# Performance work log

Measured on AMD Instinct MI355X. Metric: run time of the kernel, lower is better.

## Reference

```python
import jax, jax.numpy as jnp
import numpy as np

B, D, HW, C = 256, 128, 36, 64  # batch, proj_dim, spatial side, num classes
EPS = 1e-4


def setup_inputs() -> dict:
    key = jax.random.key(0)
    k1, k2 = jax.random.split(key)
    x = jax.random.normal(k1, (B, D, HW, HW), dtype=jnp.float32)
    class_map = jax.random.randint(k2, (B, HW, HW), 0, C, dtype=jnp.int32)
    return {"x": x, "class_map": class_map}


def reference(x, class_map):
    # Faithful to ImageParser.compute_dists: per-image group-by-class mean
    # of pixel embeddings, then per-pixel squared distance to its class mean.
    # torch.unique + one_hot over inv_idxs is equivalent to using the raw
    # class ids as segments (absent classes contribute nothing).
    b, d = x.shape[0], x.shape[1]
    n = x.shape[2] * x.shape[3]            # 36*36 = 1296
    xf = x.reshape(b, d, n)                # [B, D, N]
    cm = class_map.reshape(b, n)           # [B, N]

    onehot = jax.nn.one_hot(cm, C, dtype=xf.dtype)          # [B, N, C]
    counts = onehot.sum(axis=1)                              # [B, C]
    sums = jnp.einsum('bdn,bnc->bdc', xf, onehot)            # [B, D, C]
    means = sums / (counts[:, None, :] + EPS)                # [B, D, C]

    # gather each pixel's class mean: means[b, :, cm[b, n]] -> [B, D, N]
    idx = jnp.broadcast_to(cm[:, None, :], (b, d, n))
    gathered = jnp.take_along_axis(means, idx, axis=2)

    dists = ((xf - gathered) ** 2).mean(axis=1)              # [B, N]
    return dists[..., None]                                  # [B, N, 1] as in torch
```

## Files before the change

### kernel.cpp

```cpp
#include <hip/hip_runtime.h>

static constexpr int kB   = 256;
static constexpr int kD   = 128;
static constexpr int kN   = 1296;
static constexpr int kN4  = 324;
static constexpr int kC   = 64;
static constexpr int kDC  = 8;
static constexpr int kNCH = kD / kDC;
static constexpr int kREP = 4;
static constexpr int kT   = 384;
static constexpr float kEPS = 1e-4f;
static constexpr float kSCALE     = 131072.0f;
static constexpr float kINV_SCALE = 1.0f / 131072.0f;

__device__ __forceinline__ void fadd_glb(float* p, float v) { unsafeAtomicAdd(p, v); }

__global__ __launch_bounds__(kT) void k_fused(const float* __restrict__ x,
                                              const int*   __restrict__ cm,
                                              float* __restrict__ out)
{
    __shared__ int   isum_s[kREP][kDC][kC];
    __shared__ float means_s[kDC][kC];
    __shared__ int   cnt_s[kC];

    const int chunk = blockIdx.x;
    const int b     = blockIdx.y;
    const int tid   = threadIdx.x;
    const int rep   = (tid >> 4) & (kREP - 1);
    const int rot   = rep << 3;
    const bool act  = tid < kN4;

    for (int i = tid; i < kREP * kDC * kC; i += kT) (&isum_s[0][0][0])[i] = 0;
    if (tid < kC) cnt_s[tid] = 0;
    __syncthreads();

    int4 c0 = make_int4(0, 0, 0, 0);
    if (act) c0 = ((const int4*)(cm + (size_t)b * kN))[tid];

    const float4* xp = (const float4*)(x + ((size_t)b * kD + (size_t)chunk * kDC) * kN);
    float4 va[kDC];
#pragma unroll
    for (int dd = 0; dd < kDC; ++dd)
        va[dd] = act ? xp[(size_t)dd * kN4 + tid] : make_float4(0.f, 0.f, 0.f, 0.f);

    if (act) {
        atomicAdd(&cnt_s[c0.x], 1);
        atomicAdd(&cnt_s[c0.y], 1);
        atomicAdd(&cnt_s[c0.z], 1);
        atomicAdd(&cnt_s[c0.w], 1);
        const int sx = (c0.x + rot) & (kC - 1);
        const int sy = (c0.y + rot) & (kC - 1);
        const int sz = (c0.z + rot) & (kC - 1);
        const int sw = (c0.w + rot) & (kC - 1);
#pragma unroll
        for (int dd = 0; dd < kDC; ++dd) {
            int* s = &isum_s[rep][dd][0];
            atomicAdd(s + sx, __float2int_rn(va[dd].x * kSCALE));
            atomicAdd(s + sy, __float2int_rn(va[dd].y * kSCALE));
            atomicAdd(s + sz, __float2int_rn(va[dd].z * kSCALE));
            atomicAdd(s + sw, __float2int_rn(va[dd].w * kSCALE));
        }
    }
    __syncthreads();

    for (int i = tid; i < kDC * kC; i += kT) {
        const int dd = i >> 6;
        const int c  = i & (kC - 1);
        int s = isum_s[0][dd][c];
#pragma unroll
        for (int r = 1; r < kREP; ++r)
            s += isum_s[r][dd][(c + (r << 3)) & (kC - 1)];
        means_s[dd][c] = (float)s * kINV_SCALE / ((float)cnt_s[c] + kEPS);
    }
    __syncthreads();

    if (act) {
        float a0 = 0.f, a1 = 0.f, a2 = 0.f, a3 = 0.f;
#pragma unroll
        for (int dd = 0; dd < kDC; ++dd) {
            const float* m = &means_s[dd][0];
            const float d0 = va[dd].x - m[c0.x];
            const float d1 = va[dd].y - m[c0.y];
            const float d2 = va[dd].z - m[c0.z];
            const float d3 = va[dd].w - m[c0.w];
            a0 += d0 * d0; a1 += d1 * d1; a2 += d2 * d2; a3 += d3 * d3;
        }
        const float inv = 1.0f / (float)kD;
        float* ob = out + (size_t)b * kN + 4 * (size_t)tid;
        fadd_glb(ob + 0, a0 * inv);
        fadd_glb(ob + 1, a1 * inv);
        fadd_glb(ob + 2, a2 * inv);
        fadd_glb(ob + 3, a3 * inv);
    }
}

__global__ __launch_bounds__(kT) void k_stream(const float* __restrict__ x,
                                               float* __restrict__ ws)
{
    const int tid = threadIdx.x;
    if (tid >= kN4) return;
    const int chunk = blockIdx.x;
    const int b     = blockIdx.y;
    const float4* xp = (const float4*)(x + ((size_t)b * kD + (size_t)chunk * kDC) * kN);
    float a = 0.f;
#pragma unroll
    for (int dd = 0; dd < kDC; ++dd) {
        const float4 v = xp[(size_t)dd * kN4 + tid];
        a += v.x + v.y + v.z + v.w;
    }
    ws[((size_t)b * kNCH + chunk) * kN4 + tid] = a;
}

extern "C" void kernel_launch(void* const* d_in, const int* in_sizes, int n_in,
                              void* d_out, int out_size, void* d_ws, size_t ws_size,
                              hipStream_t stream) {
    const float* x   = (const float*)d_in[0];
    const int*   cm  = (const int*)d_in[1];
    float*       out = (float*)d_out;
    float*       ws  = (float*)d_ws;

    hipMemsetAsync(d_out, 0, (size_t)out_size * sizeof(float), stream);

    dim3 grid(kNCH, kB);
    k_fused<<<grid, kT, 0, stream>>>(x, cm, out);
    k_stream<<<grid, kT, 0, stream>>>(x, ws);
}
```

Before: 277.1 us.

## Replace global float atomics with per-chunk partials and a reduce kernel; drop redundant stream kernel

The fused kernel now writes its per-chunk squared-distance partials as float4 stores into a workspace buffer instead of doing global float atomic adds. A new small kernel sums the 16 chunk partials and applies the 1/D scale. This removes the output memset, the global atomics, and the extra kernel that re-read all of x into an unused workspace. Shared-memory zeroing is moved after the x loads and vectorised so it can overlap the load latency. The cost is an extra partial buffer write and read plus one more kernel launch.

```diff
diff --git a/kernel.cpp b/kernel.cpp
--- a/kernel.cpp
+++ b/kernel.cpp
@@ -13,11 +13,10 @@
 static constexpr float kSCALE     = 131072.0f;
 static constexpr float kINV_SCALE = 1.0f / 131072.0f;
 
-__device__ __forceinline__ void fadd_glb(float* p, float v) { unsafeAtomicAdd(p, v); }
 
 __global__ __launch_bounds__(kT) void k_fused(const float* __restrict__ x,
                                               const int*   __restrict__ cm,
-                                              float* __restrict__ out)
+                                              float* __restrict__ part)
 {
     __shared__ int   isum_s[kREP][kDC][kC];
     __shared__ float means_s[kDC][kC];
@@ -30,10 +29,6 @@
     const int rot   = rep << 3;
     const bool act  = tid < kN4;
 
-    for (int i = tid; i < kREP * kDC * kC; i += kT) (&isum_s[0][0][0])[i] = 0;
-    if (tid < kC) cnt_s[tid] = 0;
-    __syncthreads();
-
     int4 c0 = make_int4(0, 0, 0, 0);
     if (act) c0 = ((const int4*)(cm + (size_t)b * kN))[tid];
 
@@ -42,6 +37,11 @@
 #pragma unroll
     for (int dd = 0; dd < kDC; ++dd)
         va[dd] = act ? xp[(size_t)dd * kN4 + tid] : make_float4(0.f, 0.f, 0.f, 0.f);
+
+    int4* z = (int4*)&isum_s[0][0][0];
+    for (int i = tid; i < (kREP * kDC * kC) / 4; i += kT) z[i] = make_int4(0, 0, 0, 0);
+    if (tid < kC) cnt_s[tid] = 0;
+    __syncthreads();
 
     if (act) {
         atomicAdd(&cnt_s[c0.x], 1);
@@ -85,43 +85,41 @@
             const float d3 = va[dd].w - m[c0.w];
             a0 += d0 * d0; a1 += d1 * d1; a2 += d2 * d2; a3 += d3 * d3;
         }
-        const float inv = 1.0f / (float)kD;
-        float* ob = out + (size_t)b * kN + 4 * (size_t)tid;
-        fadd_glb(ob + 0, a0 * inv);
-        fadd_glb(ob + 1, a1 * inv);
-        fadd_glb(ob + 2, a2 * inv);
-        fadd_glb(ob + 3, a3 * inv);
+        float4 o; o.x = a0; o.y = a1; o.z = a2; o.w = a3;
+        float* pb = part + ((size_t)chunk * kB + b) * kN;
+        ((float4*)pb)[tid] = o;
     }
 }
 
-__global__ __launch_bounds__(kT) void k_stream(const float* __restrict__ x,
-                                               float* __restrict__ ws)
+__global__ __launch_bounds__(256) void k_reduce(const float* __restrict__ part,
+                                                float* __restrict__ out)
 {
-    const int tid = threadIdx.x;
-    if (tid >= kN4) return;
-    const int chunk = blockIdx.x;
-    const int b     = blockIdx.y;
-    const float4* xp = (const float4*)(x + ((size_t)b * kD + (size_t)chunk * kDC) * kN);
-    float a = 0.f;
+    const size_t n4_total = (size_t)kB * kN / 4;
+    const size_t i = (size_t)blockIdx.x * 256 + threadIdx.x;
+    if (i >= n4_total) return;
+
+    float4 a = ((const float4*)part)[i];
 #pragma unroll
-    for (int dd = 0; dd < kDC; ++dd) {
-        const float4 v = xp[(size_t)dd * kN4 + tid];
-        a += v.x + v.y + v.z + v.w;
+    for (int c = 1; c < kNCH; ++c) {
+        const float4 p = ((const float4*)part)[(size_t)c * n4_total + i];
+        a.x += p.x; a.y += p.y; a.z += p.z; a.w += p.w;
     }
-    ws[((size_t)b * kNCH + chunk) * kN4 + tid] = a;
+    const float inv = 1.0f / (float)kD;
+    a.x *= inv; a.y *= inv; a.z *= inv; a.w *= inv;
+    ((float4*)out)[i] = a;
 }
 
 extern "C" void kernel_launch(void* const* d_in, const int* in_sizes, int n_in,
                               void* d_out, int out_size, void* d_ws, size_t ws_size,
                               hipStream_t stream) {
-    const float* x   = (const float*)d_in[0];
-    const int*   cm  = (const int*)d_in[1];
-    float*       out = (float*)d_out;
-    float*       ws  = (float*)d_ws;
-
-    hipMemsetAsync(d_out, 0, (size_t)out_size * sizeof(float), stream);
+    const float* x    = (const float*)d_in[0];
+    const int*   cm   = (const int*)d_in[1];
+    float*       out  = (float*)d_out;
+    float*       part = (float*)d_ws;
 
     dim3 grid(kNCH, kB);
-    k_fused<<<grid, kT, 0, stream>>>(x, cm, out);
-    k_stream<<<grid, kT, 0, stream>>>(x, ws);
+    k_fused<<<grid, kT, 0, stream>>>(x, cm, part);
+
+    const int n4_total = kB * kN / 4;
+    k_reduce<<<(n4_total + 255) / 256, 256, 0, stream>>>(part, out);
 }
```

Result: faster. 242.3 us (-12.5%).
